# Performance work log

Hardware: AMD Instinct MI355X
Metric: run time of the kernel (lower is better)

## Reference

```python
import jax, jax.numpy as jnp
import numpy as np

RADIUS = 0.4
NSAMPLE = 32


def setup_inputs() -> dict:
    key = jax.random.key(0)
    ks = jax.random.split(key, 6)
    B, N, C = 2, 16384, 64
    xyz = jax.random.normal(ks[0], (B, N, 3), jnp.float32)
    features = jax.random.normal(ks[1], (B, C, N), jnp.float32)

    def w(k, i, o):
        return jax.random.normal(k, (i, o), jnp.float32) * (1.0 / np.sqrt(i))

    W1 = w(ks[2], C + 3, 64)
    W2 = w(ks[3], 64, 64)
    W3 = w(ks[4], 64, 128)
    return {
        "xyz": xyz, "features": features,
        "W1": W1, "b1": jnp.zeros((64,), jnp.float32),
        "W2": W2, "b2": jnp.zeros((64,), jnp.float32),
        "W3": W3, "b3": jnp.zeros((128,), jnp.float32),
        "npoint": 4096,
    }


def ball_query(xyz, new_xyz, radius, nsample):
    """xyz [B,N,3], new_xyz [B,S,3] -> neighbor idx [B,S,nsample] int32.
    Replicates pointnet2 ball_query: first `nsample` points (in index order)
    within `radius` of each centroid; empty slots filled with the first hit
    (0 if no point is in range)."""
    N = xyz.shape[1]
    # squared distances [B,S,N] via ||a||^2 + ||b||^2 - 2 a.b
    d2 = (jnp.sum(new_xyz * new_xyz, -1)[:, :, None]
          + jnp.sum(xyz * xyz, -1)[:, None, :]
          - 2.0 * jnp.einsum('bsc,bnc->bsn', new_xyz, xyz))
    cand = jnp.where(d2 < radius * radius,
                     jnp.arange(N, dtype=jnp.int32), jnp.int32(N))
    neg_topk, _ = jax.lax.top_k(-cand, nsample)  # nsample smallest indices
    idx = -neg_topk
    first = idx[..., :1]
    idx = jnp.where(idx == N, first, idx)  # pad with first valid neighbor
    idx = jnp.where(idx == N, 0, idx)      # no neighbor at all -> 0
    return idx


def reference(xyz, features, W1, b1, W2, b2, W3, b3, npoint):
    B = xyz.shape[0]
    # sample_method=None, keep_first_half=False -> idx = arange(npoint)
    new_xyz = xyz[:, :npoint]                        # [B,S,3]
    idx = ball_query(jax.lax.stop_gradient(xyz),
                     jax.lax.stop_gradient(new_xyz), RADIUS, NSAMPLE)
    # group: gather neighbors, re-center xyz, concat features (use_xyz=True)
    grouped_xyz = jax.vmap(lambda p, i: p[i])(xyz, idx) - new_xyz[:, :, None]  # [B,S,K,3]
    feats_nc = features.transpose(0, 2, 1)           # [B,N,C]
    grouped_f = jax.vmap(lambda f, i: f[i])(feats_nc, idx)  # [B,S,K,C]
    g = jnp.concatenate([grouped_xyz, grouped_f], axis=-1)  # [B,S,K,3+C]
    # shared MLP (1x1 convs + ReLU)
    h = jax.nn.relu(jnp.einsum('bskc,cd->bskd', g, W1) + b1)
    h = jax.nn.relu(jnp.einsum('bskc,cd->bskd', h, W2) + b2)
    h = jax.nn.relu(jnp.einsum('bskc,cd->bskd', h, W3) + b3)
    new_features = jnp.max(h, axis=2).transpose(0, 2, 1)    # [B,128,S]
    samp_idx = jnp.tile(jnp.arange(npoint, dtype=jnp.int32), (B, 1))
    return new_xyz, new_features, samp_idx
```

## Files before the change

### kernel.cpp

```cpp
#include <hip/hip_runtime.h>

#define BB 2
#define NN 16384
#define CC 64
#define SS 4096
#define KK 32
#define R2 0.16f

#define GD   24
#define GC   (GD * GD * GD)
#define CAPC 112
#define CAP  512
#define CAPL (CAP / 64)

typedef __bf16 bf16x8 __attribute__((ext_vector_type(8)));
typedef float  f32x4  __attribute__((ext_vector_type(4)));

#define MFMA(a, b, c) __builtin_amdgcn_mfma_f32_16x16x32_bf16((a), (b), (c), 0, 0, 0)

static __device__ __forceinline__ ushort f2bf(float f) {
    __bf16 h = (__bf16)f;
    return *(ushort*)&h;
}

static __device__ __forceinline__ int cellc(float x) {
    int i = (int)floorf(x * 2.5f + 12.0f);
    return i < 0 ? 0 : (i > GD - 1 ? GD - 1 : i);
}

#define WS_PTS4   0
#define WS_FEAT   524288
#define WS_W1T    4718592
#define WS_W2T    4730880
#define WS_W3T    4739072
#define WS_CNT    4755456
#define WS_LIST   4866048

#define T_PTS   (BB * NN)
#define T_W1    (T_PTS + 64 * 96)
#define T_W2    (T_W1 + 64 * 64)
#define T_W3    (T_W2 + 128 * 64)
#define T_NXYZ  (T_W3 + BB * SS * 3)
#define T_SIDX  (T_NXYZ + BB * SS)
#define T_ALL   (T_SIDX + BB * NN * 8)

__global__ __launch_bounds__(256) void prep_kernel(
        const float* __restrict__ xyz, const float* __restrict__ feat,
        const float* __restrict__ W1, const float* __restrict__ W2,
        const float* __restrict__ W3,
        float4* __restrict__ pts4, ushort* __restrict__ feat_nc,
        ushort* __restrict__ W1t, ushort* __restrict__ W2t,
        ushort* __restrict__ W3t,
        float* __restrict__ out_xyz, float* __restrict__ out_sidx,
        uint* __restrict__ counts, int* __restrict__ list) {
    const int t = blockIdx.x * 256 + threadIdx.x;
    if (t < T_PTS) {
        const float* p = xyz + (size_t)t * 3;
        const float x = p[0], y = p[1], z = p[2];
        pts4[t] = make_float4(x, y, z, x * x + y * y + z * z);
        const int cell = (cellc(z) * GD + cellc(y)) * GD + cellc(x);
        const int b = t >> 14, n = t & (NN - 1);
        const uint rank = atomicAdd(&counts[(size_t)b * GC + cell], 1u);
        if (rank < CAPC)
            list[((size_t)b * GC + cell) * CAPC + rank] = n;
    } else if (t < T_W1) {
        const int i = t - T_PTS;
        const int n = i / 96, k = i - n * 96;
        float v = 0.0f;
        if (k < 64) v = W1[(3 + k) * 64 + n];
        else if (k < 67) v = W1[(k - 64) * 64 + n];
        W1t[n * 96 + k] = f2bf(v);
    } else if (t < T_W2) {
        const int i = t - T_W1;
        const int n = i >> 6, k = i & 63;
        W2t[n * 64 + k] = f2bf(W2[k * 64 + n]);
    } else if (t < T_W3) {
        const int i = t - T_W2;
        const int n = i >> 6, k = i & 63;
        W3t[n * 64 + k] = f2bf(W3[k * 128 + n]);
    } else if (t < T_NXYZ) {
        const int i = t - T_W3;
        const int b = i / (SS * 3), j = i - b * (SS * 3);
        out_xyz[i] = xyz[(size_t)b * NN * 3 + j];
    } else if (t < T_SIDX) {
        const int i = t - T_NXYZ;
        out_sidx[i] = (float)(i & (SS - 1));
    } else if (t < T_ALL) {
        const int j = t - T_SIDX;
        const int nl = j >> 3, c8 = j & 7;
        const int b = nl >> 14, n = nl & (NN - 1);
        const float* fb = feat + (size_t)b * CC * NN + n;
        uint u[4];
        #pragma unroll
        for (int q = 0; q < 4; ++q) {
            const float f0 = fb[(size_t)(c8 * 8 + 2 * q) * NN];
            const float f1 = fb[(size_t)(c8 * 8 + 2 * q + 1) * NN];
            u[q] = (uint)f2bf(f0) | ((uint)f2bf(f1) << 16);
        }
        *(uint4*)(feat_nc + (size_t)nl * 64 + c8 * 8) = make_uint4(u[0], u[1], u[2], u[3]);
    }
}

__global__ __launch_bounds__(256, 2) void fused_kernel(
        const float4* __restrict__ pts4, const ushort* __restrict__ feat_nc,
        const uint* __restrict__ counts, const int* __restrict__ list,
        const ushort* __restrict__ W1t, const ushort* __restrict__ W2t,
        const ushort* __restrict__ W3t,
        const float* __restrict__ b1, const float* __restrict__ b2,
        const float* __restrict__ b3, float* __restrict__ out_feat) {
    const int w = threadIdx.x >> 6, lane = threadIdx.x & 63;
    const int quad = lane >> 4, mrow = lane & 15;
    const int m = lane & 31, half = lane >> 5;

    __shared__ __align__(16) ushort ldsA[4][32 * 104];
    __shared__ float stage[128][5];
    ushort* gbuf = ldsA[w];
    int* hit = (int*)gbuf;

    const int xcd = blockIdx.x & 7;
    const int slot = blockIdx.x >> 3;
    const int b = xcd >> 2;
    const int s0 = ((xcd & 3) * 256 + slot) * 4;
    const int s = s0 + w;

    const float4* pb = pts4 + (size_t)b * NN;
    const ushort* fbase = feat_nc + (size_t)b * NN * 64;
    const unsigned long long ltmask = (1ull << lane) - 1ull;

    {
        const float4 c = pb[s];
        const int cx = cellc(c.x), cy = cellc(c.y), cz = cellc(c.z);
        const uint* cntb = counts + (size_t)b * GC;
        const int* listb = list + (size_t)b * GC * CAPC;

        int pre[28], A[27];
        pre[0] = 0;
        #pragma unroll
        for (int e = 0; e < 27; ++e) {
            const int z = cz + e / 9 - 1;
            const int y = cy + (e / 3) % 3 - 1;
            const int x = cx + e % 3 - 1;
            const bool ok = ((unsigned)z < GD) && ((unsigned)y < GD) && ((unsigned)x < GD);
            const int ci = (z * GD + y) * GD + x;
            int cn = ok ? (int)cntb[ci] : 0;
            cn = cn < CAPC ? cn : CAPC;
            A[e] = ci * CAPC - pre[e];
            pre[e + 1] = pre[e] + cn;
        }
        const int tot = pre[27];

        int cnt = 0;
        for (int g0 = 0; g0 < tot; g0 += 64) {
            const int g = g0 + lane;
            int adj = A[0];
            #pragma unroll
            for (int k = 1; k < 27; ++k) adj = (g >= pre[k]) ? A[k] : adj;
            const bool act = g < tot;
            const int id = act ? listb[g + adj] : 0;
            const float4 p = pb[id];
            const float d = c.w + p.w - 2.0f * (c.x * p.x + c.y * p.y + c.z * p.z);
            const bool h = act && (d < R2);
            const unsigned long long mk = __ballot(h);
            if (h) {
                const int pp = cnt + __popcll(mk & ltmask);
                if (pp < CAP) hit[pp] = id;
            }
            cnt += (int)__popcll(mk);
        }

        if (cnt > KK) {
            const int stored = cnt < CAP ? cnt : CAP;
            int v[CAPL];
            #pragma unroll
            for (int j = 0; j < CAPL; ++j) {
                const int q = j * 64 + lane;
                const int val = hit[q];
                v[j] = (q < stored) ? val : 0x7fffffff;
            }
            int lo = 0, hi = NN - 1;
            while (lo < hi) {
                const int mid = (lo + hi) >> 1;
                int cle = 0;
                #pragma unroll
                for (int j = 0; j < CAPL; ++j)
                    if (j * 64 < stored)
                        cle += (int)__popcll(__ballot(v[j] <= mid));
                if (cle >= KK) hi = mid; else lo = mid + 1;
            }
            int pos = 0;
            #pragma unroll
            for (int j = 0; j < CAPL; ++j) {
                if (j * 64 < stored) {
                    const bool sel = v[j] <= lo;
                    const unsigned long long mk = __ballot(sel);
                    if (sel) hit[pos + __popcll(mk & ltmask)] = v[j];
                    pos += (int)__popcll(mk);
                }
            }
        } else if (lane < KK) {
            const int vv = (cnt == 0) ? 0 : ((lane < cnt) ? hit[lane] : hit[0]);
            hit[lane] = vv;
        }
    }

    {
        const int sid = hit[m];
        const ushort* src = fbase + (size_t)sid * 64 + half * 32;
        ushort* dst = gbuf + m * 104 + half * 32;
        uint4 rows[4];
        #pragma unroll
        for (int i = 0; i < 4; ++i) rows[i] = *(const uint4*)(src + i * 8);
        const float4 p = pb[sid];
        const float4 cc = pb[s];
        #pragma unroll
        for (int i = 0; i < 4; ++i) *(uint4*)(dst + i * 8) = rows[i];
        if (half == 0) {
            bf16x8 rel = {(__bf16)(p.x - cc.x), (__bf16)(p.y - cc.y),
                          (__bf16)(p.z - cc.z), (__bf16)0.f,
                          (__bf16)0.f, (__bf16)0.f, (__bf16)0.f, (__bf16)0.f};
            *(bf16x8*)(gbuf + m * 104 + 64) = rel;
            *(uint4*)(gbuf + m * 104 + 88) = make_uint4(0, 0, 0, 0);
        } else {
            *(uint4*)(gbuf + m * 104 + 72) = make_uint4(0, 0, 0, 0);
            *(uint4*)(gbuf + m * 104 + 80) = make_uint4(0, 0, 0, 0);
        }
    }

    {
        f32x4 acc[2][4];
        #pragma unroll
        for (int nt = 0; nt < 4; ++nt) {
            const float bv = b1[nt * 16 + mrow];
            acc[0][nt] = (f32x4){bv, bv, bv, bv};
            acc[1][nt] = acc[0][nt];
        }
        #pragma unroll
        for (int ks = 0; ks < 3; ++ks) {
            const bf16x8 a0 = *(const bf16x8*)(gbuf + mrow * 104 + ks * 32 + quad * 8);
            const bf16x8 a1 = *(const bf16x8*)(gbuf + (16 + mrow) * 104 + ks * 32 + quad * 8);
            #pragma unroll
            for (int nt = 0; nt < 4; ++nt) {
                const bf16x8 wf = *(const bf16x8*)(W1t + (nt * 16 + mrow) * 96 + ks * 32 + quad * 8);
                acc[0][nt] = MFMA(a0, wf, acc[0][nt]);
                acc[1][nt] = MFMA(a1, wf, acc[1][nt]);
            }
        }
        #pragma unroll
        for (int mt = 0; mt < 2; ++mt)
            #pragma unroll
            for (int nt = 0; nt < 4; ++nt)
                #pragma unroll
                for (int r = 0; r < 4; ++r)
                    gbuf[(mt * 16 + quad * 4 + r) * 104 + nt * 16 + mrow] =
                        f2bf(fmaxf(acc[mt][nt][r], 0.0f));
    }

    {
        f32x4 acc[2][4];
        #pragma unroll
        for (int nt = 0; nt < 4; ++nt) {
            const float bv = b2[nt * 16 + mrow];
            acc[0][nt] = (f32x4){bv, bv, bv, bv};
            acc[1][nt] = acc[0][nt];
        }
        #pragma unroll
        for (int ks = 0; ks < 2; ++ks) {
            const bf16x8 a0 = *(const bf16x8*)(gbuf + mrow * 104 + ks * 32 + quad * 8);
            const bf16x8 a1 = *(const bf16x8*)(gbuf + (16 + mrow) * 104 + ks * 32 + quad * 8);
            #pragma unroll
            for (int nt = 0; nt < 4; ++nt) {
                const bf16x8 wf = *(const bf16x8*)(W2t + (nt * 16 + mrow) * 64 + ks * 32 + quad * 8);
                acc[0][nt] = MFMA(a0, wf, acc[0][nt]);
                acc[1][nt] = MFMA(a1, wf, acc[1][nt]);
            }
        }
        #pragma unroll
        for (int mt = 0; mt < 2; ++mt)
            #pragma unroll
            for (int nt = 0; nt < 4; ++nt)
                #pragma unroll
                for (int r = 0; r < 4; ++r)
                    gbuf[(mt * 16 + quad * 4 + r) * 104 + nt * 16 + mrow] =
                        f2bf(fmaxf(acc[mt][nt][r], 0.0f));
    }

    #pragma unroll
    for (int nh = 0; nh < 2; ++nh) {
        f32x4 acc[2][4];
        #pragma unroll
        for (int ntl = 0; ntl < 4; ++ntl) {
            const float bv = b3[(nh * 4 + ntl) * 16 + mrow];
            acc[0][ntl] = (f32x4){bv, bv, bv, bv};
            acc[1][ntl] = acc[0][ntl];
        }
        #pragma unroll
        for (int ks = 0; ks < 2; ++ks) {
            const bf16x8 a0 = *(const bf16x8*)(gbuf + mrow * 104 + ks * 32 + quad * 8);
            const bf16x8 a1 = *(const bf16x8*)(gbuf + (16 + mrow) * 104 + ks * 32 + quad * 8);
            #pragma unroll
            for (int ntl = 0; ntl < 4; ++ntl) {
                const bf16x8 wf = *(const bf16x8*)(
                    W3t + ((nh * 4 + ntl) * 16 + mrow) * 64 + ks * 32 + quad * 8);
                acc[0][ntl] = MFMA(a0, wf, acc[0][ntl]);
                acc[1][ntl] = MFMA(a1, wf, acc[1][ntl]);
            }
        }
        #pragma unroll
        for (int ntl = 0; ntl < 4; ++ntl) {
            const f32x4 v0 = acc[0][ntl], v1 = acc[1][ntl];
            float mx = fmaxf(fmaxf(v0[0], v0[1]), fmaxf(v0[2], v0[3]));
            mx = fmaxf(mx, fmaxf(fmaxf(v1[0], v1[1]), fmaxf(v1[2], v1[3])));
            mx = fmaxf(mx, __shfl_xor(mx, 16));
            mx = fmaxf(mx, __shfl_xor(mx, 32));
            mx = fmaxf(mx, 0.0f);
            if (quad == 0) stage[(nh * 4 + ntl) * 16 + mrow][w] = mx;
        }
    }
    __syncthreads();

    {
        const int ch = threadIdx.x & 127;
        const int hf = threadIdx.x >> 7;
        float* dst = out_feat + ((size_t)b * 128 + ch) * SS + s0 + hf * 2;
        *(float2*)dst = make_float2(stage[ch][hf * 2], stage[ch][hf * 2 + 1]);
    }
}

extern "C" void kernel_launch(void* const* d_in, const int* in_sizes, int n_in,
                              void* d_out, int out_size, void* d_ws, size_t ws_size,
                              hipStream_t stream) {
    const float* xyz  = (const float*)d_in[0];
    const float* feat = (const float*)d_in[1];
    const float* W1   = (const float*)d_in[2];
    const float* b1   = (const float*)d_in[3];
    const float* W2   = (const float*)d_in[4];
    const float* b2   = (const float*)d_in[5];
    const float* W3   = (const float*)d_in[6];
    const float* b3   = (const float*)d_in[7];

    float* out      = (float*)d_out;
    float* out_xyz  = out;
    float* out_feat = out + (size_t)BB * SS * 3;
    float* out_sidx = out_feat + (size_t)BB * 128 * SS;

    char* ws = (char*)d_ws;
    float4* pts4    = (float4*)(ws + WS_PTS4);
    ushort* feat_nc = (ushort*)(ws + WS_FEAT);
    ushort* W1t     = (ushort*)(ws + WS_W1T);
    ushort* W2t     = (ushort*)(ws + WS_W2T);
    ushort* W3t     = (ushort*)(ws + WS_W3T);
    uint*   counts  = (uint*)(ws + WS_CNT);
    int*    list    = (int*)(ws + WS_LIST);

    hipMemsetAsync(counts, 0, (size_t)BB * GC * 4, stream);
    prep_kernel<<<(T_ALL + 255) / 256, 256, 0, stream>>>(
        xyz, feat, W1, W2, W3, pts4, feat_nc, W1t, W2t, W3t, out_xyz, out_sidx,
        counts, list);
    fused_kernel<<<BB * SS / 4, 256, 0, stream>>>(pts4, feat_nc, counts, list,
                                                  W1t, W2t, W3t, b1, b2, b3,
                                                  out_feat);
}
```

Before: 148.5 us.

## Store cell-sorted point coords and transpose features through an LDS tile

The grid build now writes each point's float4 (xyz plus squared norm) into a cell-ordered array alongside the index list. The ball-query scan then reads coordinates contiguously instead of doing a dependent gather through the index, and loads the index only for hits. Separately, the feature transpose to bf16 NC layout now goes through a shared-memory tile so both global reads and writes are coalesced. The cost is an extra, mostly sparse workspace buffer of float4 per cell slot and more prep-kernel writes.

```diff
diff --git a/kernel.cpp b/kernel.cpp
--- a/kernel.cpp
+++ b/kernel.cpp
@@ -35,6 +35,7 @@
 #define WS_W3T    4739072
 #define WS_CNT    4755456
 #define WS_LIST   4866048
+#define WS_LPTS   17252352
 
 #define T_PTS   (BB * NN)
 #define T_W1    (T_PTS + 64 * 96)
@@ -42,7 +43,8 @@
 #define T_W3    (T_W2 + 128 * 64)
 #define T_NXYZ  (T_W3 + BB * SS * 3)
 #define T_SIDX  (T_NXYZ + BB * SS)
-#define T_ALL   (T_SIDX + BB * NN * 8)
+#define FEAT_B0 (T_SIDX / 256)
+#define NBLK    (FEAT_B0 + BB * (NN / 32))
 
 __global__ __launch_bounds__(256) void prep_kernel(
         const float* __restrict__ xyz, const float* __restrict__ feat,
@@ -52,17 +54,45 @@
         ushort* __restrict__ W1t, ushort* __restrict__ W2t,
         ushort* __restrict__ W3t,
         float* __restrict__ out_xyz, float* __restrict__ out_sidx,
-        uint* __restrict__ counts, int* __restrict__ list) {
+        uint* __restrict__ counts, int* __restrict__ list,
+        float4* __restrict__ lpts) {
+    if (blockIdx.x >= FEAT_B0) {
+        __shared__ float tile[64][33];
+        const int g = blockIdx.x - FEAT_B0;
+        const int b = g >> 9, n0 = (g & 511) << 5;
+        const int t = threadIdx.x;
+        const float* fb = feat + (size_t)b * CC * NN + n0;
+        #pragma unroll
+        for (int cc = 0; cc < 8; ++cc) {
+            const int c = cc * 8 + (t >> 5);
+            tile[c][t & 31] = fb[(size_t)c * NN + (t & 31)];
+        }
+        __syncthreads();
+        const int p = t >> 3, c8 = t & 7;
+        uint u[4];
+        #pragma unroll
+        for (int q = 0; q < 4; ++q) {
+            u[q] = (uint)f2bf(tile[c8 * 8 + 2 * q][p]) |
+                   ((uint)f2bf(tile[c8 * 8 + 2 * q + 1][p]) << 16);
+        }
+        *(uint4*)(feat_nc + ((size_t)b * NN + n0 + p) * 64 + c8 * 8) =
+            make_uint4(u[0], u[1], u[2], u[3]);
+        return;
+    }
     const int t = blockIdx.x * 256 + threadIdx.x;
     if (t < T_PTS) {
         const float* p = xyz + (size_t)t * 3;
         const float x = p[0], y = p[1], z = p[2];
-        pts4[t] = make_float4(x, y, z, x * x + y * y + z * z);
+        const float4 pv = make_float4(x, y, z, x * x + y * y + z * z);
+        pts4[t] = pv;
         const int cell = (cellc(z) * GD + cellc(y)) * GD + cellc(x);
         const int b = t >> 14, n = t & (NN - 1);
         const uint rank = atomicAdd(&counts[(size_t)b * GC + cell], 1u);
-        if (rank < CAPC)
-            list[((size_t)b * GC + cell) * CAPC + rank] = n;
+        if (rank < CAPC) {
+            const size_t slot = ((size_t)b * GC + cell) * CAPC + rank;
+            list[slot] = n;
+            lpts[slot] = pv;
+        }
     } else if (t < T_W1) {
         const int i = t - T_PTS;
         const int n = i / 96, k = i - n * 96;
@@ -85,25 +115,13 @@
     } else if (t < T_SIDX) {
         const int i = t - T_NXYZ;
         out_sidx[i] = (float)(i & (SS - 1));
-    } else if (t < T_ALL) {
-        const int j = t - T_SIDX;
-        const int nl = j >> 3, c8 = j & 7;
-        const int b = nl >> 14, n = nl & (NN - 1);
-        const float* fb = feat + (size_t)b * CC * NN + n;
-        uint u[4];
-        #pragma unroll
-        for (int q = 0; q < 4; ++q) {
-            const float f0 = fb[(size_t)(c8 * 8 + 2 * q) * NN];
-            const float f1 = fb[(size_t)(c8 * 8 + 2 * q + 1) * NN];
-            u[q] = (uint)f2bf(f0) | ((uint)f2bf(f1) << 16);
-        }
-        *(uint4*)(feat_nc + (size_t)nl * 64 + c8 * 8) = make_uint4(u[0], u[1], u[2], u[3]);
     }
 }
 
 __global__ __launch_bounds__(256, 2) void fused_kernel(
         const float4* __restrict__ pts4, const ushort* __restrict__ feat_nc,
         const uint* __restrict__ counts, const int* __restrict__ list,
+        const float4* __restrict__ lpts,
         const ushort* __restrict__ W1t, const ushort* __restrict__ W2t,
         const ushort* __restrict__ W3t,
         const float* __restrict__ b1, const float* __restrict__ b2,
@@ -132,6 +150,7 @@
         const int cx = cellc(c.x), cy = cellc(c.y), cz = cellc(c.z);
         const uint* cntb = counts + (size_t)b * GC;
         const int* listb = list + (size_t)b * GC * CAPC;
+        const float4* lptsb = lpts + (size_t)b * GC * CAPC;
 
         int pre[28], A[27];
         pre[0] = 0;
@@ -156,14 +175,14 @@
             #pragma unroll
             for (int k = 1; k < 27; ++k) adj = (g >= pre[k]) ? A[k] : adj;
             const bool act = g < tot;
-            const int id = act ? listb[g + adj] : 0;
-            const float4 p = pb[id];
+            const int ga = act ? (g + adj) : 0;
+            const float4 p = lptsb[ga];
             const float d = c.w + p.w - 2.0f * (c.x * p.x + c.y * p.y + c.z * p.z);
             const bool h = act && (d < R2);
             const unsigned long long mk = __ballot(h);
             if (h) {
                 const int pp = cnt + __popcll(mk & ltmask);
-                if (pp < CAP) hit[pp] = id;
+                if (pp < CAP) hit[pp] = listb[ga];
             }
             cnt += (int)__popcll(mk);
         }
@@ -351,12 +370,13 @@
     ushort* W3t     = (ushort*)(ws + WS_W3T);
     uint*   counts  = (uint*)(ws + WS_CNT);
     int*    list    = (int*)(ws + WS_LIST);
+    float4* lpts    = (float4*)(ws + WS_LPTS);
 
     hipMemsetAsync(counts, 0, (size_t)BB * GC * 4, stream);
-    prep_kernel<<<(T_ALL + 255) / 256, 256, 0, stream>>>(
+    prep_kernel<<<NBLK, 256, 0, stream>>>(
         xyz, feat, W1, W2, W3, pts4, feat_nc, W1t, W2t, W3t, out_xyz, out_sidx,
-        counts, list);
+        counts, list, lpts);
     fused_kernel<<<BB * SS / 4, 256, 0, stream>>>(pts4, feat_nc, counts, list,
-                                                  W1t, W2t, W3t, b1, b2, b3,
-                                                  out_feat);
-}
+                                                  lpts, W1t, W2t, W3t,
+                                                  b1, b2, b3, out_feat);
+}
```

Measured after the change: 144.6 us. 1.03x faster.
